# Kernel optimization log

Hardware: AMD Instinct MI355X
Metric: run time of the kernel (lower is better)

Reference implementation:

```python
import jax, jax.numpy as jnp
import numpy as np


def setup_inputs() -> dict:
    key = jax.random.key(0)
    k1, k2 = jax.random.split(key)
    x = jax.random.normal(k1, (8, 2048, 512), dtype=jnp.float32)
    codebook = jax.random.normal(k2, (8192, 512), dtype=jnp.float32)
    return {"x": x, "codebook": codebook}


def reference(x, codebook):
    # x: [B, S, D]; codebook: [K, D]
    B, S, D = x.shape
    flat_x = x.reshape(-1, D)  # [N, D], N = B*S
    # argmin over L2 distance == argmin over squared L2 distance:
    x_sq = jnp.sum(flat_x * flat_x, axis=-1, keepdims=True)        # [N, 1]
    c_sq = jnp.sum(codebook * codebook, axis=-1)                   # [K]
    dots = jnp.einsum('nd,kd->nk', flat_x, codebook)               # [N, K]
    dist_sq = x_sq - 2.0 * dots + c_sq[None, :]                    # [N, K]
    indices = jnp.argmin(dist_sq, axis=1)                          # [N]
    quantized = jnp.take(codebook, indices, axis=0)                # [N, D]
    return quantized.reshape(x.shape)
```

## Files before the change

kernel.cpp:

```cpp
#include <hip/hip_runtime.h>
#include <cstdint>

constexpr int DD = 512;
constexpr int KK = 8192;
constexpr int NROWS = 16384;
#define MARGIN 1.0f

constexpr size_t AX_ELEMS = (size_t)NROWS * DD;
constexpr size_t BF_ELEMS = (size_t)KK * DD;
constexpr size_t KEY_ELEMS = (size_t)NROWS * 128;
constexpr size_t WS_NEEDED =
    AX_ELEMS * 2 + BF_ELEMS * 2 + (size_t)KK * 4 + KEY_ELEMS * 8;

typedef __attribute__((ext_vector_type(8))) short short8v;
typedef __attribute__((ext_vector_type(8))) _Float16 half8v;
typedef __attribute__((ext_vector_type(4))) float floatx4;
typedef unsigned long long ull;

__device__ __forceinline__ ull umin64(ull a, ull b) { return a < b ? a : b; }
__device__ __forceinline__ uint32_t fsort(float f) {
  uint32_t u = __float_as_uint(f);
  return (u & 0x80000000u) ? ~u : (u | 0x80000000u);
}
__device__ __forceinline__ float funsort(uint32_t u) {
  uint32_t f = (u & 0x80000000u) ? (u ^ 0x80000000u) : ~u;
  return __uint_as_float(f);
}

__device__ __forceinline__ void gl_lds16(const ushort* g, ushort* l) {
  __builtin_amdgcn_global_load_lds(
      (const __attribute__((address_space(1))) unsigned int*)g,
      (__attribute__((address_space(3))) unsigned int*)l, 16, 0, 0);
}

__device__ __forceinline__ float pairwise128_sq(const float* __restrict__ p) {
#pragma clang fp contract(off)
  float r[8];
  {
    float4 a = ((const float4*)p)[0];
    float4 b = ((const float4*)p)[1];
    r[0] = a.x * a.x; r[1] = a.y * a.y; r[2] = a.z * a.z; r[3] = a.w * a.w;
    r[4] = b.x * b.x; r[5] = b.y * b.y; r[6] = b.z * b.z; r[7] = b.w * b.w;
  }
  for (int i = 2; i < 32; i += 2) {
    float4 a = ((const float4*)p)[i];
    float4 b = ((const float4*)p)[i + 1];
    r[0] = r[0] + a.x * a.x; r[1] = r[1] + a.y * a.y;
    r[2] = r[2] + a.z * a.z; r[3] = r[3] + a.w * a.w;
    r[4] = r[4] + b.x * b.x; r[5] = r[5] + b.y * b.y;
    r[6] = r[6] + b.z * b.z; r[7] = r[7] + b.w * b.w;
  }
  return ((r[0] + r[1]) + (r[2] + r[3])) + ((r[4] + r[5]) + (r[6] + r[7]));
}

__global__ __launch_bounds__(256)
void cast16_kernel(const float* __restrict__ src, ushort* __restrict__ dst) {
  int idx = blockIdx.x * 256 + threadIdx.x;
  float4 v = *(const float4*)(src + (size_t)idx * 4);
  ushort h[4];
  float vv[4] = {v.x, v.y, v.z, v.w};
#pragma unroll
  for (int i = 0; i < 4; ++i) h[i] = __builtin_bit_cast(ushort, (_Float16)vv[i]);
  *(ushort4*)(dst + (size_t)idx * 4) = make_ushort4(h[0], h[1], h[2], h[3]);
}

__global__ __launch_bounds__(256)
void csq_kernel(const float* __restrict__ CB, float* __restrict__ csq) {
  __shared__ float cblk[64][4];
  int t = threadIdx.x;
  int r0 = blockIdx.x * 64;
  int row = t >> 2, blk = t & 3;
  cblk[row][blk] = pairwise128_sq(CB + (size_t)(r0 + row) * DD + blk * 128);
  __syncthreads();
  if (t < 64) {
#pragma clang fp contract(off)
    csq[r0 + t] = (cblk[t][0] + cblk[t][1]) + (cblk[t][2] + cblk[t][3]);
  }
}

__global__ __launch_bounds__(256, 4)
void vq_screen16_kernel(const ushort* __restrict__ Axp, const ushort* __restrict__ Bfp,
                        const float* __restrict__ csq, ull* __restrict__ keys) {
  __shared__ ushort AS[128 * 64];
  __shared__ ushort BS[128 * 64];
  __shared__ ull mb[128][2][2];

  const int t = threadIdx.x;
  const int L = t & 63;
  const int w = t >> 6;
  const int wr = (w >> 1) * 64, wc = (w & 1) * 64;
  const int seg = L >> 4;
  const int l15 = L & 15;

  const int bid = blockIdx.x;
  const int xcd = bid & 7;
  const int loc = bid >> 3;
  const int ri  = loc & 7;
  const int cbi = (loc >> 3) & 7;
  const int rg  = loc >> 6;
  const int rb  = rg * 8 + ri;
  const int cb  = xcd * 8 + cbi;
  const size_t r0 = (size_t)rb * 128, c0 = (size_t)cb * 128;

  const int lrow = L >> 3;
  const int lgr = (L & 7) ^ lrow;
  const ushort* srcA0 = Axp + (r0 + w * 32 + lrow) * DD + lgr * 8;
  const ushort* srcB0 = Bfp + (c0 + w * 32 + lrow) * DD + lgr * 8;

  int aoff[2][4], boff[2][4];
#pragma unroll
  for (int s = 0; s < 2; ++s) {
    const int kcol = s * 4 + (L >> 4);
#pragma unroll
    for (int m = 0; m < 4; ++m) {
      const int rl = wr + m * 16 + l15;
      aoff[s][m] = rl * 64 + ((kcol * 8) ^ ((rl & 7) * 8));
      const int cl = wc + m * 16 + l15;
      boff[s][m] = cl * 64 + ((kcol * 8) ^ ((cl & 7) * 8));
    }
  }

  floatx4 acc[4][4];
#pragma unroll
  for (int m = 0; m < 4; ++m)
#pragma unroll
    for (int n = 0; n < 4; ++n) acc[m][n] = (floatx4){0.f, 0.f, 0.f, 0.f};

  for (int kc = 0; kc < 8; ++kc) {
    if (kc) __syncthreads();
#pragma unroll
    for (int j = 0; j < 4; ++j) {
      gl_lds16(srcA0 + (size_t)j * 8 * DD + kc * 64, &AS[(w * 32 + j * 8) * 64]);
      gl_lds16(srcB0 + (size_t)j * 8 * DD + kc * 64, &BS[(w * 32 + j * 8) * 64]);
    }
    __syncthreads();

#pragma unroll
    for (int s = 0; s < 2; ++s) {
      half8v af[4], bf[4];
#pragma unroll
      for (int m = 0; m < 4; ++m) af[m] = *(const half8v*)&AS[aoff[s][m]];
#pragma unroll
      for (int n = 0; n < 4; ++n) bf[n] = *(const half8v*)&BS[boff[s][n]];
#pragma unroll
      for (int m = 0; m < 4; ++m)
#pragma unroll
        for (int n = 0; n < 4; ++n)
          acc[m][n] = __builtin_amdgcn_mfma_f32_16x16x32_f16(af[m], bf[n], acc[m][n], 0, 0, 0);
    }
  }

  float cq[4];
#pragma unroll
  for (int n = 0; n < 4; ++n) cq[n] = csq[c0 + wc + n * 16 + l15];
  const float INF = __builtin_inff();

#pragma unroll
  for (int m = 0; m < 4; ++m) {
#pragma unroll
    for (int i = 0; i < 4; ++i) {
      float q0 = __builtin_fmaf(-2.f, acc[m][0][i], cq[0]);
      float q1 = __builtin_fmaf(-2.f, acc[m][1][i], cq[1]);
      float q2 = __builtin_fmaf(-2.f, acc[m][2][i], cq[2]);
      float q3 = __builtin_fmaf(-2.f, acc[m][3][i], cq[3]);
      const int rl = wr + m * 16 + seg * 4 + i;

      float qm = fminf(fminf(q0, q1), fminf(q2, q3));
#pragma unroll
      for (int mask = 1; mask <= 8; mask <<= 1) qm = fminf(qm, __shfl_xor(qm, mask, 64));
      int n1 = (q0 == qm) ? 0 : (q1 == qm) ? 1 : (q2 == qm) ? 2 : (q3 == qm) ? 3 : 4;
      ull bal = __ballot(n1 < 4);
      int fl = __ffsll((bal >> (seg * 16)) & 0xFFFFull) - 1;
      const bool own1 = (l15 == fl);
      if (own1) {
        int col = (int)c0 + wc + n1 * 16 + l15;
        mb[rl][w & 1][0] = ((ull)fsort(qm) << 32) | (uint32_t)col;
      }
      float e0 = q0, e1 = q1, e2 = q2, e3 = q3;
      if (own1) {
        if (n1 == 0) e0 = INF; else if (n1 == 1) e1 = INF;
        else if (n1 == 2) e2 = INF; else e3 = INF;
      }
      float q2m = fminf(fminf(e0, e1), fminf(e2, e3));
#pragma unroll
      for (int mask = 1; mask <= 8; mask <<= 1) q2m = fminf(q2m, __shfl_xor(q2m, mask, 64));
      int n2 = (e0 == q2m) ? 0 : (e1 == q2m) ? 1 : (e2 == q2m) ? 2 : (e3 == q2m) ? 3 : 4;
      ull bal2 = __ballot(n2 < 4);
      int fl2 = __ffsll((bal2 >> (seg * 16)) & 0xFFFFull) - 1;
      if (l15 == fl2) {
        int col = (int)c0 + wc + n2 * 16 + l15;
        mb[rl][w & 1][1] = ((ull)fsort(q2m) << 32) | (uint32_t)col;
      }
    }
  }
  __syncthreads();
  if (t < 128) {
    ull a1 = mb[t][0][0], a2 = mb[t][0][1];
    ull b1 = mb[t][1][0], b2 = mb[t][1][1];
    ull k1, k2;
    if (a1 < b1) { k1 = a1; k2 = umin64(a2, b1); }
    else { k1 = b1; k2 = umin64(b2, a1); }
    keys[(r0 + t) * 128 + cb * 2 + 0] = k1;
    keys[(r0 + t) * 128 + cb * 2 + 1] = k2;
  }
}

__global__ __launch_bounds__(256)
void vq_reduce_kernel(const float* __restrict__ X, const float* __restrict__ CB,
                      const float* __restrict__ csq, const ull* __restrict__ keys,
                      float* __restrict__ out) {
  __shared__ int bidx[4];
  const int t = threadIdx.x;
  const int L = t & 63;
  const int w = t >> 6;
  const size_t row = (size_t)blockIdx.x * 4 + w;
  ulonglong2 kk = *(const ulonglong2*)(keys + row * 128 + L * 2);

  ull kmin = umin64(kk.x, kk.y);
#pragma unroll
  for (int m = 32; m; m >>= 1) {
    ull o = __shfl_xor(kmin, m, 64);
    if (o < kmin) kmin = o;
  }
  const float qcut = funsort((uint32_t)(kmin >> 32)) + MARGIN;

  const bool q0 = funsort((uint32_t)(kk.x >> 32)) <= qcut;
  const bool q1 = funsort((uint32_t)(kk.y >> 32)) <= qcut;
  const ull b0 = __ballot(q0);
  const ull b1 = __ballot(q1);
  const int total = __popcll(b0) + __popcll(b1);

  int winner;
  if (total <= 1) {
    winner = (int)(kmin & 0xffffffffu);
  } else {
    const float* xp = X + row * DD;
    const float4 xa = ((const float4*)xp)[L * 2];
    const float4 xb = ((const float4*)xp)[L * 2 + 1];
    ull bestE = ~0ull;
#pragma unroll
    for (int pass = 0; pass < 2; ++pass) {
      ull mask = pass ? b1 : b0;
      while (mask) {
        const int lane = __ffsll(mask) - 1;
        mask &= mask - 1;
        const ull key = __shfl(pass ? kk.y : kk.x, lane, 64);
        const int idx = (int)(key & 0xffffffffu);
        const float* cp = CB + (size_t)idx * DD;
        const float4 ca = ((const float4*)cp)[L * 2];
        const float4 cbv = ((const float4*)cp)[L * 2 + 1];
        float p = 0.f;
        p = __builtin_fmaf(xa.x, ca.x, p);
        p = __builtin_fmaf(xa.y, ca.y, p);
        p = __builtin_fmaf(xa.z, ca.z, p);
        p = __builtin_fmaf(xa.w, ca.w, p);
        p = __builtin_fmaf(xb.x, cbv.x, p);
        p = __builtin_fmaf(xb.y, cbv.y, p);
        p = __builtin_fmaf(xb.z, cbv.z, p);
        p = __builtin_fmaf(xb.w, cbv.w, p);
#pragma unroll
        for (int m = 32; m; m >>= 1) p += __shfl_xor(p, m, 64);
        const float q = csq[idx] - 2.0f * p;
        const ull ek = ((ull)fsort(q) << 32) | (uint32_t)idx;
        bestE = umin64(bestE, ek);
      }
    }
    winner = (int)(bestE & 0xffffffffu);
  }
  if (L == 0) bidx[w] = winner;
  __syncthreads();

  const size_t r0 = (size_t)blockIdx.x * 4;
#pragma unroll
  for (int it = 0; it < 2; ++it) {
    int idx = t + it * 256;
    int rw = idx >> 7, c4 = idx & 127;
    float4 v = *(const float4*)(CB + (size_t)bidx[rw] * DD + c4 * 4);
    *(float4*)(out + (r0 + rw) * DD + c4 * 4) = v;
  }
}

constexpr int FBM = 128, FBN = 128, FBK = 32, FNT = 256;
constexpr int FKSPLIT = 4;
constexpr int FKPB = KK / FKSPLIT;

__global__ __launch_bounds__(FNT)
void vq_partial_kernel(const float* __restrict__ X, const float* __restrict__ CB,
                       float* __restrict__ keyout) {
  __shared__ float Xs[FBK][FBM + 4];
  __shared__ float Cs[FBK][FBN + 4];
  __shared__ float xblk[FBM][4];
  __shared__ float cblk[FBN][4];
  __shared__ float xsq[FBM];
  __shared__ float csq[FBN];

  const int t = threadIdx.x;
  const int tx = t & 15;
  const int ty = t >> 4;
  const int bid = blockIdx.x;
  const int xcd = bid & 7;
  const int loc = bid >> 3;
  const int ksplit = xcd >> 1;
  const int rowblk = (xcd & 1) * 64 + loc;
  const long r0 = (long)rowblk * FBM;
  const int kbase = ksplit * FKPB;

#pragma unroll
  for (int it = 0; it < 2; ++it) {
    int task = t + it * FNT;
    int row = task >> 2, blk = task & 3;
    xblk[row][blk] = pairwise128_sq(X + (r0 + row) * DD + blk * 128);
  }
  __syncthreads();
  if (t < FBM) {
#pragma clang fp contract(off)
    xsq[t] = (xblk[t][0] + xblk[t][1]) + (xblk[t][2] + xblk[t][3]);
  }

  uint64_t bestKey[8];
#pragma unroll
  for (int i = 0; i < 8; ++i) bestKey[i] = ~0ull;

  float4 xr[4], cr[4];
  for (int kt = 0; kt < FKPB / FBN; ++kt) {
    const int k0 = kbase + kt * FBN;
    __syncthreads();
#pragma unroll
    for (int it = 0; it < 4; ++it) {
      int idx = t + it * FNT;
      int row = idx >> 3, dg = (idx & 7) * 4;
      xr[it] = *(const float4*)(X + (r0 + row) * DD + dg);
      cr[it] = *(const float4*)(CB + (long)(k0 + row) * DD + dg);
    }
#pragma unroll
    for (int it = 0; it < 2; ++it) {
      int task = t + it * FNT;
      int cw = task >> 2, blk = task & 3;
      cblk[cw][blk] = pairwise128_sq(CB + (long)(k0 + cw) * DD + blk * 128);
    }
    __syncthreads();
    if (t < FBN) {
#pragma clang fp contract(off)
      csq[t] = (cblk[t][0] + cblk[t][1]) + (cblk[t][2] + cblk[t][3]);
    }

    float acc[8][8];
#pragma unroll
    for (int i = 0; i < 8; ++i)
#pragma unroll
      for (int j = 0; j < 8; ++j) acc[i][j] = 0.0f;

    for (int dc = 0; dc < DD; dc += FBK) {
#pragma unroll
      for (int it = 0; it < 4; ++it) {
        int idx = t + it * FNT;
        int row = idx >> 3, dg = (idx & 7) * 4;
        Xs[dg + 0][row] = xr[it].x; Xs[dg + 1][row] = xr[it].y;
        Xs[dg + 2][row] = xr[it].z; Xs[dg + 3][row] = xr[it].w;
        Cs[dg + 0][row] = cr[it].x; Cs[dg + 1][row] = cr[it].y;
        Cs[dg + 2][row] = cr[it].z; Cs[dg + 3][row] = cr[it].w;
      }
      if (dc + FBK < DD) {
#pragma unroll
        for (int it = 0; it < 4; ++it) {
          int idx = t + it * FNT;
          int row = idx >> 3, dg = (idx & 7) * 4 + dc + FBK;
          xr[it] = *(const float4*)(X + (r0 + row) * DD + dg);
          cr[it] = *(const float4*)(CB + (long)(k0 + row) * DD + dg);
        }
      }
      __syncthreads();
#pragma unroll 4
      for (int d = 0; d < FBK; ++d) {
        const float4 xa0 = *(const float4*)&Xs[d][ty * 4];
        const float4 xa1 = *(const float4*)&Xs[d][64 + ty * 4];
        const float4 cb0 = *(const float4*)&Cs[d][tx * 4];
        const float4 cb1 = *(const float4*)&Cs[d][64 + tx * 4];
        const float xv[8] = {xa0.x, xa0.y, xa0.z, xa0.w, xa1.x, xa1.y, xa1.z, xa1.w};
        const float cv[8] = {cb0.x, cb0.y, cb0.z, cb0.w, cb1.x, cb1.y, cb1.z, cb1.w};
#pragma unroll
        for (int i = 0; i < 8; ++i)
#pragma unroll
          for (int j = 0; j < 8; ++j)
            acc[i][j] = __builtin_fmaf(xv[i], cv[j], acc[i][j]);
      }
      __syncthreads();
    }
    {
#pragma clang fp contract(off)
#pragma unroll
      for (int i = 0; i < 8; ++i) {
        int rl = (i < 4) ? (ty * 4 + i) : (64 + ty * 4 + (i - 4));
        float xsv = xsq[rl];
#pragma unroll
        for (int j = 0; j < 8; ++j) {
          int cl = (j < 4) ? (tx * 4 + j) : (64 + tx * 4 + (j - 4));
          float m = 2.0f * acc[i][j];
          float t1 = xsv - m;
          float dist = t1 + csq[cl];
          uint64_t key = ((uint64_t)fsort(dist) << 32) | (uint32_t)(k0 + cl);
          if (key < bestKey[i]) bestKey[i] = key;
        }
      }
    }
  }
#pragma unroll
  for (int i = 0; i < 8; ++i) {
    ull k = bestKey[i];
#pragma unroll
    for (int m = 1; m <= 8; m <<= 1) {
      ull o = __shfl_xor(k, m, 64);
      if (o < k) k = o;
    }
    if (tx == 0) {
      int rl = (i < 4) ? (ty * 4 + i) : (64 + ty * 4 + (i - 4));
      *(ull*)(keyout + (r0 + rl) * DD + ksplit * 2) = k;
    }
  }
}

__global__ __launch_bounds__(FNT)
void vq_reduce_gather_kernel(const float* __restrict__ CB, float* __restrict__ out) {
  __shared__ int bidx[32];
  const int t = threadIdx.x;
  const long r0 = (long)blockIdx.x * 32;
  if (t < 32) {
    const ull* kp = (const ull*)(out + (r0 + t) * DD);
    ull k = kp[0];
#pragma unroll
    for (int s = 1; s < FKSPLIT; ++s) k = umin64(k, kp[s]);
    bidx[t] = (int)(k & 0xffffffffu);
  }
  __syncthreads();
#pragma unroll
  for (int it = 0; it < 16; ++it) {
    int idx = t + it * FNT;
    int row = idx >> 7, c4 = idx & 127;
    const float4 v = *(const float4*)(CB + (long)bidx[row] * DD + c4 * 4);
    *(float4*)(out + (r0 + row) * DD + c4 * 4) = v;
  }
}

extern "C" void kernel_launch(void* const* d_in, const int* in_sizes, int n_in,
                              void* d_out, int out_size, void* d_ws, size_t ws_size,
                              hipStream_t stream) {
  const float* X = (const float*)d_in[0];
  const float* CB = (const float*)d_in[1];
  float* out = (float*)d_out;

  if (ws_size >= WS_NEEDED) {
    ushort* Axp = (ushort*)d_ws;
    ushort* Bfp = Axp + AX_ELEMS;
    float* csqp = (float*)(Bfp + BF_ELEMS);
    ull* keys = (ull*)(csqp + KK);
    hipLaunchKernelGGL(cast16_kernel, dim3(NROWS * DD / 4 / 256), dim3(256), 0, stream, X, Axp);
    hipLaunchKernelGGL(cast16_kernel, dim3(KK * DD / 4 / 256), dim3(256), 0, stream, CB, Bfp);
    hipLaunchKernelGGL(csq_kernel, dim3(KK / 64), dim3(256), 0, stream, CB, csqp);
    hipLaunchKernelGGL(vq_screen16_kernel, dim3((NROWS / 128) * (KK / 128)), dim3(256), 0, stream,
                       Axp, Bfp, csqp, keys);
    hipLaunchKernelGGL(vq_reduce_kernel, dim3(NROWS / 4), dim3(256), 0, stream,
                       X, CB, csqp, keys, out);
  } else {
    hipLaunchKernelGGL(vq_partial_kernel, dim3(512), dim3(FNT), 0, stream, X, CB, out);
    hipLaunchKernelGGL(vq_reduce_gather_kernel, dim3(NROWS / 32), dim3(FNT), 0, stream, CB, out);
  }
}
```

Measured before the change: 256.0 us.

## Double-buffer LDS tiles to overlap global loads with MFMA compute

Splits the A and B shared-memory tiles into two buffers so the load for the next K chunk is issued before the MFMAs on the current chunk run. Explicit vmcnt waits and raw barriers replace __syncthreads so loads stay in flight during compute. This doubles LDS use, and the launch bound is lowered from 4 to 2 blocks per CU, which can cost occupancy.

```diff
diff --git a/kernel.cpp b/kernel.cpp
--- a/kernel.cpp
+++ b/kernel.cpp
@@ -78,11 +78,11 @@
   }
 }
 
-__global__ __launch_bounds__(256, 4)
+__global__ __launch_bounds__(256, 2)
 void vq_screen16_kernel(const ushort* __restrict__ Axp, const ushort* __restrict__ Bfp,
                         const float* __restrict__ csq, ull* __restrict__ keys) {
-  __shared__ ushort AS[128 * 64];
-  __shared__ ushort BS[128 * 64];
+  __shared__ ushort AS[2][128 * 64];
+  __shared__ ushort BS[2][128 * 64];
   __shared__ ull mb[128][2][2];
 
   const int t = threadIdx.x;
@@ -110,7 +110,7 @@
   int aoff[2][4], boff[2][4];
 #pragma unroll
   for (int s = 0; s < 2; ++s) {
-    const int kcol = s * 4 + (L >> 4);
+    const int kcol = s * 4 + seg;
 #pragma unroll
     for (int m = 0; m < 4; ++m) {
       const int rl = wr + m * 16 + l15;
@@ -126,29 +126,51 @@
 #pragma unroll
     for (int n = 0; n < 4; ++n) acc[m][n] = (floatx4){0.f, 0.f, 0.f, 0.f};
 
+#define STAGE(KC, BUF)                                                          \
+  {                                                                             \
+    _Pragma("unroll") for (int j = 0; j < 4; ++j) {                             \
+      gl_lds16(srcA0 + (size_t)j * 8 * DD + (KC) * 64,                          \
+               &AS[BUF][(w * 32 + j * 8) * 64]);                                \
+      gl_lds16(srcB0 + (size_t)j * 8 * DD + (KC) * 64,                          \
+               &BS[BUF][(w * 32 + j * 8) * 64]);                                \
+    }                                                                           \
+  }
+
+  STAGE(0, 0);
+  asm volatile("s_waitcnt vmcnt(0)" ::: "memory");
+  __builtin_amdgcn_s_barrier();
+  __builtin_amdgcn_sched_barrier(0);
+
+  int buf = 0;
   for (int kc = 0; kc < 8; ++kc) {
-    if (kc) __syncthreads();
-#pragma unroll
-    for (int j = 0; j < 4; ++j) {
-      gl_lds16(srcA0 + (size_t)j * 8 * DD + kc * 64, &AS[(w * 32 + j * 8) * 64]);
-      gl_lds16(srcB0 + (size_t)j * 8 * DD + kc * 64, &BS[(w * 32 + j * 8) * 64]);
-    }
-    __syncthreads();
+    if (kc < 7) {
+      STAGE(kc + 1, buf ^ 1);
+      asm volatile("s_waitcnt vmcnt(8)" ::: "memory");
+    } else {
+      asm volatile("s_waitcnt vmcnt(0)" ::: "memory");
+    }
+    __builtin_amdgcn_s_barrier();
+    __builtin_amdgcn_sched_barrier(0);
 
 #pragma unroll
     for (int s = 0; s < 2; ++s) {
       half8v af[4], bf[4];
 #pragma unroll
-      for (int m = 0; m < 4; ++m) af[m] = *(const half8v*)&AS[aoff[s][m]];
-#pragma unroll
-      for (int n = 0; n < 4; ++n) bf[n] = *(const half8v*)&BS[boff[s][n]];
+      for (int m = 0; m < 4; ++m) af[m] = *(const half8v*)&AS[buf][aoff[s][m]];
+#pragma unroll
+      for (int n = 0; n < 4; ++n) bf[n] = *(const half8v*)&BS[buf][boff[s][n]];
 #pragma unroll
       for (int m = 0; m < 4; ++m)
 #pragma unroll
         for (int n = 0; n < 4; ++n)
           acc[m][n] = __builtin_amdgcn_mfma_f32_16x16x32_f16(af[m], bf[n], acc[m][n], 0, 0, 0);
     }
-  }
+    asm volatile("s_waitcnt lgkmcnt(0)" ::: "memory");
+    __builtin_amdgcn_s_barrier();
+    __builtin_amdgcn_sched_barrier(0);
+    buf ^= 1;
+  }
+#undef STAGE
 
   float cq[4];
 #pragma unroll
```

After: 323.5 us. 26.3% more time.
